# Performance work log

Measured on AMD Instinct MI355X. Metric: run time of the kernel, lower is better.

Reference implementation:

```python
import jax, jax.numpy as jnp
import numpy as np


def _conv1x1(w, b, x):
    # 1x1 Conv2d == channel matmul: w [O,C], x [B,C,H,W] -> [B,O,H,W]
    return jnp.einsum('oc,bchw->bohw', w, x) + b[None, :, None, None]


def setup_inputs() -> dict:
    key = jax.random.key(0)
    ks = jax.random.split(key, 9)
    C = 512
    B, H, W = 8, 32, 32
    s = 0.02
    return {
        'x': jax.random.normal(ks[0], (B, C, H, W), dtype=jnp.float32),
        'wq': jax.random.normal(ks[1], (C, C), dtype=jnp.float32) * s,
        'bq': jax.random.normal(ks[2], (C,), dtype=jnp.float32) * s,
        'wk': jax.random.normal(ks[3], (C, C), dtype=jnp.float32) * s,
        'bk': jax.random.normal(ks[4], (C,), dtype=jnp.float32) * s,
        'wv': jax.random.normal(ks[5], (C, C), dtype=jnp.float32) * s,
        'bv': jax.random.normal(ks[6], (C,), dtype=jnp.float32) * s,
        'wo': jax.random.normal(ks[7], (C, C), dtype=jnp.float32) * s,
        'bo': jax.random.normal(ks[8], (C,), dtype=jnp.float32) * s,
        'heads': 8,
    }


def reference(x, wq, bq, wk, bk, wv, bv, wo, bo, heads):
    B, C, H, W = x.shape
    N = H * W
    d = C // heads
    scale = jnp.asarray(d, x.dtype) ** 0.5

    vx = _conv1x1(wv, bv, x)                       # value(x), reused for residual
    Q = _conv1x1(wq, bq, x).reshape(B, heads, d, N)
    K = _conv1x1(wk, bk, x).reshape(B, heads, d, N)
    V = vx.reshape(B, heads, d, N)

    attn = jax.nn.softmax(jnp.einsum('bhcn,bhcm->bhnm', Q, K) / scale, axis=-1)
    attn_out = jnp.einsum('bhnm,bhcm->bhcn', attn, V).reshape(B, C, H, W)

    out = attn_out + vx                            # residual uses value(x)
    return _conv1x1(wo, bo, out)
```

## Files before the change

### kernel.cpp

```cpp
#include <hip/hip_runtime.h>
#include <cstdint>
#include <cmath>

#define B_ 8
#define C_ 512
#define N_ 1024
#define H_ 8
#define D_ 64


using u16 = unsigned short;

typedef __bf16 bf16x8 __attribute__((ext_vector_type(8)));
typedef float  f32x4  __attribute__((ext_vector_type(4)));
typedef unsigned short us8 __attribute__((ext_vector_type(8)));

#if __has_builtin(__builtin_amdgcn_exp2f)
#define EXP2(x) __builtin_amdgcn_exp2f(x)
#else
#define EXP2(x) exp2f(x)
#endif

#define QSCALE 0.1803368801111244f


__device__ __forceinline__ float b2f(u16 u) {
    return __uint_as_float(((uint32_t)u) << 16);
}
__device__ __forceinline__ u16 f2b(float f) {
    uint32_t x = __float_as_uint(f);
    return (u16)((x + 0x7fffu + ((x >> 16) & 1u)) >> 16);
}
__device__ __forceinline__ u16 f2bt(float f) {
    return (u16)(__float_as_uint(f) >> 16);
}
__device__ __forceinline__ float sf(float f) {
    return (fabsf(f) < 1e30f) ? f : 0.0f;
}
__device__ __forceinline__ u16 sf2b(float f) { return f2b(sf(f)); }

__device__ __forceinline__ void gl16(const void* g, const void* l) {
    __builtin_amdgcn_global_load_lds(
        (const __attribute__((address_space(1))) uint32_t*)g,
        (__attribute__((address_space(3))) uint32_t*)(uint32_t)(uintptr_t)l,
        16, 0, 0);
}

__device__ __forceinline__ us8 ldwf(const float* W, size_t idx) {
    const float* p = W + idx;
    float4 a = *(const float4*)p, b = *(const float4*)(p + 4);
    us8 pk;
    pk[0] = sf2b(a.x); pk[1] = sf2b(a.y); pk[2] = sf2b(a.z); pk[3] = sf2b(a.w);
    pk[4] = sf2b(b.x); pk[5] = sf2b(b.y); pk[6] = sf2b(b.z); pk[7] = sf2b(b.w);
    return pk;
}


__global__ __launch_bounds__(256) void k_pre(const float* __restrict__ x,
                                             u16* __restrict__ xt,
                                             const float* __restrict__ wq,
                                             const float* __restrict__ wk,
                                             const float* __restrict__ wv,
                                             const float* __restrict__ wo,
                                             u16* __restrict__ wb) {
    const int tid = threadIdx.x;
    const int nb = blockIdx.x, cb = blockIdx.y, b = blockIdx.z;
    if (b == 8) {
        if (wb == nullptr) return;
        int base = (cb * 16 + nb) * 256 + tid;
#pragma unroll
        for (int i = 0; i < 8; ++i) {
            int idx = base + i * 32768;
            int m = idx >> 16;
            int off = (idx & 65535) << 2;
            const float* src = (m == 0) ? wq : (m == 1) ? wk : (m == 2) ? wv : wo;
            float4 v = *(const float4*)&src[off];
            ushort4 w;
            w.x = sf2b(v.x); w.y = sf2b(v.y); w.z = sf2b(v.z); w.w = sf2b(v.w);
            *(ushort4*)&wb[(m << 18) + off] = w;
        }
        return;
    }
    __shared__ __align__(16) u16 t[64][72];
#pragma unroll
    for (int i = 0; i < 4; ++i) {
        int q = tid + i * 256;
        int row = q >> 4, cg = q & 15;
        float4 v = *(const float4*)&x[((size_t)(b * C_ + cb * 64 + row) << 10) + nb * 64 + cg * 4];
        ushort4 w;
        w.x = sf2b(v.x); w.y = sf2b(v.y); w.z = sf2b(v.z); w.w = sf2b(v.w);
        *(ushort4*)&t[row][cg * 4] = w;
    }
    __syncthreads();
#pragma unroll
    for (int i = 0; i < 4; ++i) {
        int q = tid + i * 256;
        int nrow = q >> 4, cg = q & 15;
        ushort4 w;
        w.x = t[cg * 4 + 0][nrow];
        w.y = t[cg * 4 + 1][nrow];
        w.z = t[cg * 4 + 2][nrow];
        w.w = t[cg * 4 + 3][nrow];
        *(ushort4*)&xt[((size_t)(b * N_ + nb * 64 + nrow) << 9) + cb * 64 + cg * 4] = w;
    }
}


template<bool WB>
__global__ __launch_bounds__(256) void k_proj_t(
    const u16* __restrict__ xt,
    const void* __restrict__ wq, const float* __restrict__ bq,
    const void* __restrict__ wk, const float* __restrict__ bk,
    const void* __restrict__ wv, const float* __restrict__ bv,
    u16* __restrict__ qt, u16* __restrict__ kt,
    u16* __restrict__ v,  u16* __restrict__ vxt) {
    __shared__ __align__(16) u16 lA[128 * 64];
    __shared__ __align__(16) u16 lB[128 * 64];
    const int tid = threadIdx.x;
    const int op = blockIdx.z >> 3, b = blockIdx.z & 7;
    const int n0 = blockIdx.x * 128, o0 = blockIdx.y * 128;
    const void*  W  = (op == 0) ? wq : (op == 1) ? wk : wv;
    const float* BI = (op == 0) ? bq : (op == 1) ? bk : bv;
    const u16* A = xt + ((size_t)b << 19);
    const int lane = tid & 63, wave = tid >> 6;
    const int wm = (wave >> 1) * 64, wn = (wave & 1) * 64;
    const int l15 = lane & 15, lg = lane >> 4;
    const int xs = (l15 & 7) << 3;

    f32x4 acc[4][4];
    const f32x4 vzero = {0.f, 0.f, 0.f, 0.f};
#pragma unroll
    for (int i = 0; i < 4; ++i)
#pragma unroll
        for (int j = 0; j < 4; ++j) acc[i][j] = vzero;

    us8 ra[4], rwB[4];
    auto loadk = [&](int k0) {
#pragma unroll
        for (int p = 0; p < 4; ++p) {
            int slot = p * 256 + tid;
            int row = slot >> 3, seg = slot & 7;
            ra[p] = *(const us8*)&A[(size_t)(n0 + row) * C_ + k0 + seg * 8];
            rwB[p] = ldwf((const float*)W, (size_t)(o0 + row) * C_ + k0 + seg * 8);
        }
    };
    if constexpr (!WB) loadk(0);

    for (int k0 = 0; k0 < C_; k0 += 64) {
        __syncthreads();
        if constexpr (WB) {
            const u16* W16 = (const u16*)W;
#pragma unroll
            for (int p = 0; p < 4; ++p) {
                int slot = p * 256 + tid;
                int row = slot >> 3;
                int segs = (slot & 7) ^ (row & 7);
                int lb = (p * 256 + (tid & 192)) * 8;
                gl16(&A[(size_t)(n0 + row) * C_ + k0 + segs * 8], &lA[lb]);
                gl16(&W16[(size_t)(o0 + row) * C_ + k0 + segs * 8], &lB[lb]);
            }
        } else {
#pragma unroll
            for (int p = 0; p < 4; ++p) {
                int slot = p * 256 + tid;
                int row = slot >> 3, seg = slot & 7;
                int off = row * 64 + ((seg ^ (row & 7)) << 3);
                *(us8*)&lA[off] = ra[p];
                *(us8*)&lB[off] = rwB[p];
            }
            if (k0 + 64 < C_) loadk(k0 + 64);
        }
        __syncthreads();
#pragma unroll
        for (int kk = 0; kk < 64; kk += 32) {
            const int col = (kk + lg * 8) ^ xs;
            bf16x8 af[4], bfr[4];
#pragma unroll
            for (int i = 0; i < 4; ++i)
                af[i] = *(const bf16x8*)&lA[(wm + i * 16 + l15) * 64 + col];
#pragma unroll
            for (int j = 0; j < 4; ++j)
                bfr[j] = *(const bf16x8*)&lB[(wn + j * 16 + l15) * 64 + col];
#pragma unroll
            for (int i = 0; i < 4; ++i)
#pragma unroll
                for (int j = 0; j < 4; ++j)
                    acc[i][j] = __builtin_amdgcn_mfma_f32_16x16x32_bf16(af[i], bfr[j], acc[i][j], 0, 0, 0);
        }
    }

    if (op < 2) {
        u16* outp = (op == 0) ? qt : kt;
        const float scl = (op == 0) ? QSCALE : 1.0f;
#pragma unroll
        for (int i = 0; i < 4; ++i) {
            int nb2 = n0 + wm + i * 16 + lg * 4;
#pragma unroll
            for (int j = 0; j < 4; ++j) {
                int o = o0 + wn + j * 16 + l15;
                float bias = sf(BI[o]);
                int h = o >> 6, dl = o & 63;
                size_t base = ((size_t)b * H_ + h) << 10;
#pragma unroll
                for (int r = 0; r < 4; ++r)
                    outp[(base + nb2 + r) * D_ + dl] = f2b((acc[i][j][r] + bias) * scl);
            }
        }
    } else {
#pragma unroll
        for (int i = 0; i < 4; ++i) {
            int nb2 = n0 + wm + i * 16 + lg * 4;
#pragma unroll
            for (int j = 0; j < 4; ++j) {
                int o = o0 + wn + j * 16 + l15;
                float bias = sf(BI[o]);
                float p0 = acc[i][j][0] + bias, p1 = acc[i][j][1] + bias;
                float p2 = acc[i][j][2] + bias, p3 = acc[i][j][3] + bias;
                ushort4 pk; pk.x = f2b(p0); pk.y = f2b(p1); pk.z = f2b(p2); pk.w = f2b(p3);
                *(ushort4*)&v[((size_t)(b * C_ + o) << 10) + nb2] = pk;
                vxt[((size_t)(b * N_ + nb2 + 0) << 9) + o] = pk.x;
                vxt[((size_t)(b * N_ + nb2 + 1) << 9) + o] = pk.y;
                vxt[((size_t)(b * N_ + nb2 + 2) << 9) + o] = pk.z;
                vxt[((size_t)(b * N_ + nb2 + 3) << 9) + o] = pk.w;
            }
        }
    }
}


__global__ __launch_bounds__(256, 3) void k_attn(
    const u16* __restrict__ qt, const u16* __restrict__ kt,
    const u16* __restrict__ v,  const u16* __restrict__ vxt,
    u16* __restrict__ rt) {
    __shared__ __align__(16) u16 lK[2][64 * 64];
    __shared__ __align__(16) u16 lV[2][64 * 64];
    __shared__ __align__(16) u16 lP[4][32 * 64];
    const int tid = threadIdx.x, lane = tid & 63, wave = tid >> 6;
    const int l15 = lane & 15, lg = lane >> 4;
    const int xs = (l15 & 7) << 3;
    const int bid = blockIdx.x;
    const int qb = bid >> 6, bh = bid & 63;
    const int b = bh >> 3, h = bh & 7;
    const size_t bh_off = (size_t)bh << 16;
    const int q0 = qb * 128;
    const int nA = wave * 32;

    bf16x8 qf[2][2];
#pragma unroll
    for (int nt = 0; nt < 2; ++nt)
#pragma unroll
        for (int k = 0; k < 2; ++k)
            qf[nt][k] = *(const bf16x8*)&qt[bh_off +
                (size_t)(q0 + nA + nt * 16 + l15) * D_ + k * 32 + lg * 8];

    auto stage = [&](int mb, int buf) {
#pragma unroll
        for (int p = 0; p < 2; ++p) {
            int slot = p * 256 + tid;
            int row = slot >> 3;
            int segs = (slot & 7) ^ (row & 7);
            int lb = (p * 256 + (tid & 192)) * 8;
            gl16(&kt[bh_off + (size_t)(mb * 64 + row) * D_ + segs * 8], &lK[buf][lb]);
            gl16(&v[((size_t)(b * C_ + h * 64 + row) << 10) + mb * 64 + segs * 8], &lV[buf][lb]);
        }
    };
    stage(0, 0);
    __syncthreads();

    float L[2] = {0.f, 0.f};
    f32x4 oacc[2][4];
    const f32x4 vzero = {0.f, 0.f, 0.f, 0.f};
#pragma unroll
    for (int nt = 0; nt < 2; ++nt)
#pragma unroll
        for (int ct = 0; ct < 4; ++ct) oacc[nt][ct] = vzero;

    for (int mb = 0; mb < 16; ++mb) {
        const int cur = mb & 1;
        if (mb < 15) stage(mb + 1, cur ^ 1);
        const u16* lKc = lK[cur];
        const u16* lVc = lV[cur];

        f32x4 s[4][2];
#pragma unroll
        for (int mt = 0; mt < 4; ++mt)
#pragma unroll
            for (int nt = 0; nt < 2; ++nt) s[mt][nt] = vzero;
#pragma unroll
        for (int k = 0; k < 2; ++k) {
            const int col = (k * 32 + lg * 8) ^ xs;
            bf16x8 aK[4];
#pragma unroll
            for (int mt = 0; mt < 4; ++mt)
                aK[mt] = *(const bf16x8*)&lKc[(mt * 16 + l15) * 64 + col];
            __builtin_amdgcn_s_setprio(1);
#pragma unroll
            for (int mt = 0; mt < 4; ++mt)
#pragma unroll
                for (int nt = 0; nt < 2; ++nt)
                    s[mt][nt] = __builtin_amdgcn_mfma_f32_16x16x32_bf16(aK[mt], qf[nt][k], s[mt][nt], 0, 0, 0);
            __builtin_amdgcn_s_setprio(0);
        }

#pragma unroll
        for (int mt = 0; mt < 4; ++mt)
#pragma unroll
            for (int nt = 0; nt < 2; ++nt) {
                float p0 = EXP2(s[mt][nt][0]);
                float p1 = EXP2(s[mt][nt][1]);
                float p2 = EXP2(s[mt][nt][2]);
                float p3 = EXP2(s[mt][nt][3]);
                L[nt] += p0 + p1 + p2 + p3;
                ushort4 pk; pk.x = f2bt(p0); pk.y = f2bt(p1); pk.z = f2bt(p2); pk.w = f2bt(p3);
                *(ushort4*)&lP[wave][(nt * 16 + l15) * 64 + ((mt * 16 + lg * 4) ^ xs)] = pk;
            }

#pragma unroll
        for (int kk2 = 0; kk2 < 64; kk2 += 32) {
            const int colv = (kk2 + lg * 8) ^ xs;
            bf16x8 aP[2], bV[4];
#pragma unroll
            for (int nt = 0; nt < 2; ++nt)
                aP[nt] = *(const bf16x8*)&lP[wave][(nt * 16 + l15) * 64 + colv];
#pragma unroll
            for (int ct = 0; ct < 4; ++ct)
                bV[ct] = *(const bf16x8*)&lVc[(ct * 16 + l15) * 64 + colv];
            __builtin_amdgcn_s_setprio(1);
#pragma unroll
            for (int nt = 0; nt < 2; ++nt)
#pragma unroll
                for (int ct = 0; ct < 4; ++ct)
                    oacc[nt][ct] = __builtin_amdgcn_mfma_f32_16x16x32_bf16(aP[nt], bV[ct], oacc[nt][ct], 0, 0, 0);
            __builtin_amdgcn_s_setprio(0);
        }

        __syncthreads();
    }

#pragma unroll
    for (int nt = 0; nt < 2; ++nt) {
        float s2 = L[nt];
        s2 += __shfl_xor(s2, 16);
        s2 += __shfl_xor(s2, 32);
        L[nt] = s2;
    }

#pragma unroll
    for (int nt = 0; nt < 2; ++nt) {
        float inv[4];
#pragma unroll
        for (int r = 0; r < 4; ++r) inv[r] = 1.0f / __shfl(L[nt], lg * 4 + r);
#pragma unroll
        for (int ct = 0; ct < 4; ++ct) {
            int ch = h * 64 + ct * 16 + l15;
#pragma unroll
            for (int r = 0; r < 4; ++r) {
                int n = q0 + nA + nt * 16 + lg * 4 + r;
                size_t idx = ((size_t)(b * N_ + n) << 9) + ch;
                rt[idx] = f2b(oacc[nt][ct][r] * inv[r] + b2f(vxt[idx]));
            }
        }
    }
}


template<bool WB>
__global__ __launch_bounds__(256) void k_out_t(
    const u16* __restrict__ rt, const void* __restrict__ wo,
    const float* __restrict__ bo, float* __restrict__ out) {
    __shared__ __align__(16) u16 lA[128 * 64];
    __shared__ __align__(16) u16 lB[128 * 64];
    const int tid = threadIdx.x;
    const int b = blockIdx.z;
    const int n0 = blockIdx.x * 128, o0 = blockIdx.y * 128;
    const u16* Rb = rt + ((size_t)b << 19);
    const int lane = tid & 63, wave = tid >> 6;
    const int wm = (wave >> 1) * 64, wn = (wave & 1) * 64;
    const int l15 = lane & 15, lg = lane >> 4;
    const int xs = (l15 & 7) << 3;

    f32x4 acc[4][4];
    const f32x4 vzero = {0.f, 0.f, 0.f, 0.f};
#pragma unroll
    for (int i = 0; i < 4; ++i)
#pragma unroll
        for (int j = 0; j < 4; ++j) acc[i][j] = vzero;

    us8 rb[4], rwB[4];
    auto loadk = [&](int k0) {
#pragma unroll
        for (int p = 0; p < 4; ++p) {
            int slot = p * 256 + tid;
            int row = slot >> 3, seg = slot & 7;
            rwB[p] = ldwf((const float*)wo, (size_t)(o0 + row) * C_ + k0 + seg * 8);
            rb[p] = *(const us8*)&Rb[(size_t)(n0 + row) * C_ + k0 + seg * 8];
        }
    };
    if constexpr (!WB) loadk(0);

    for (int k0 = 0; k0 < C_; k0 += 64) {
        __syncthreads();
        if constexpr (WB) {
            const u16* W16 = (const u16*)wo;
#pragma unroll
            for (int p = 0; p < 4; ++p) {
                int slot = p * 256 + tid;
                int row = slot >> 3;
                int segs = (slot & 7) ^ (row & 7);
                int lb = (p * 256 + (tid & 192)) * 8;
                gl16(&W16[(size_t)(o0 + row) * C_ + k0 + segs * 8], &lA[lb]);
                gl16(&Rb[(size_t)(n0 + row) * C_ + k0 + segs * 8], &lB[lb]);
            }
        } else {
#pragma unroll
            for (int p = 0; p < 4; ++p) {
                int slot = p * 256 + tid;
                int row = slot >> 3, seg = slot & 7;
                int off = row * 64 + ((seg ^ (row & 7)) << 3);
                *(us8*)&lA[off] = rwB[p];
                *(us8*)&lB[off] = rb[p];
            }
            if (k0 + 64 < C_) loadk(k0 + 64);
        }
        __syncthreads();
#pragma unroll
        for (int kk = 0; kk < 64; kk += 32) {
            const int col = (kk + lg * 8) ^ xs;
            bf16x8 af[4], bfr[4];
#pragma unroll
            for (int i = 0; i < 4; ++i)
                af[i] = *(const bf16x8*)&lA[(wm + i * 16 + l15) * 64 + col];
#pragma unroll
            for (int j = 0; j < 4; ++j)
                bfr[j] = *(const bf16x8*)&lB[(wn + j * 16 + l15) * 64 + col];
#pragma unroll
            for (int i = 0; i < 4; ++i)
#pragma unroll
                for (int j = 0; j < 4; ++j)
                    acc[i][j] = __builtin_amdgcn_mfma_f32_16x16x32_bf16(af[i], bfr[j], acc[i][j], 0, 0, 0);
        }
    }

#pragma unroll
    for (int i = 0; i < 4; ++i) {
#pragma unroll
        for (int j = 0; j < 4; ++j) {
            int nn = n0 + wn + j * 16 + l15;
#pragma unroll
            for (int r = 0; r < 4; ++r) {
                int o = o0 + wm + i * 16 + lg * 4 + r;
                out[((size_t)(b * C_ + o) << 10) + nn] = acc[i][j][r] + sf(bo[o]);
            }
        }
    }
}


extern "C" void kernel_launch(void* const* d_in, const int* in_sizes, int n_in,
                              void* d_out, int out_size, void* d_ws, size_t ws_size,
                              hipStream_t stream) {
    const float* x  = (const float*)d_in[0];
    const float* wq = (const float*)d_in[1];
    const float* bq = (const float*)d_in[2];
    const float* wk = (const float*)d_in[3];
    const float* bk = (const float*)d_in[4];
    const float* wv = (const float*)d_in[5];
    const float* bv = (const float*)d_in[6];
    const float* wo = (const float*)d_in[7];
    const float* bo = (const float*)d_in[8];
    float* out = (float*)d_out;
    u16* ws = (u16*)d_ws;

    const size_t T = (size_t)B_ * C_ * N_;
    const size_t WSZ = (size_t)4 * C_ * C_;
    if (ws_size < 5 * T * sizeof(u16)) return;

    u16* xt  = ws;
    u16* qt  = ws + 1 * T;
    u16* kt  = ws + 2 * T;
    u16* vv  = ws + 3 * T;
    u16* vxt = ws + 4 * T;
    u16* rt  = xt;
    u16* wb  = ws + 5 * T;

    const bool wbfit = ws_size >= (5 * T + WSZ) * sizeof(u16);

    k_pre<<<dim3(16, 8, 9), 256, 0, stream>>>(x, xt, wq, wk, wv, wo,
                                              wbfit ? wb : (u16*)nullptr);
    if (wbfit) {
        k_proj_t<true><<<dim3(8, 4, 24), 256, 0, stream>>>(
            xt, wb, bq, wb + 262144, bk, wb + 524288, bv, qt, kt, vv, vxt);
    } else {
        k_proj_t<false><<<dim3(8, 4, 24), 256, 0, stream>>>(
            xt, wq, bq, wk, bk, wv, bv, qt, kt, vv, vxt);
    }
    k_attn<<<dim3(512), 256, 0, stream>>>(qt, kt, vv, vxt, rt);
    if (wbfit) {
        k_out_t<true><<<dim3(8, 4, 8), 256, 0, stream>>>(rt, wb + 786432, bo, out);
    } else {
        k_out_t<false><<<dim3(8, 4, 8), 256, 0, stream>>>(rt, wo, bo, out);
    }
}
```

Before: 76.31 us.

## Switch attention kernel to 32x32x16 MFMA and keep P in registers

Rewrites the attention inner loop to use 32x32x16 bf16 MFMA tiles instead of 16x16x32. The softmax probabilities are packed and redistributed across lanes with cross-half shuffles, so P no longer round-trips through LDS. That removes the lP shared buffer and its writes and reads, and reduces LDS footprint. In exchange it adds shuffle and select overhead, uses larger accumulator register tiles, and depends on the lane layout mapping being exactly right.

```diff
diff --git a/kernel.cpp b/kernel.cpp
--- a/kernel.cpp
+++ b/kernel.cpp
@@ -13,7 +13,9 @@
 
 typedef __bf16 bf16x8 __attribute__((ext_vector_type(8)));
 typedef float  f32x4  __attribute__((ext_vector_type(4)));
+typedef float  f32x16 __attribute__((ext_vector_type(16)));
 typedef unsigned short us8 __attribute__((ext_vector_type(8)));
+typedef uint32_t u32x4 __attribute__((ext_vector_type(4)));
 
 #if __has_builtin(__builtin_amdgcn_exp2f)
 #define EXP2(x) __builtin_amdgcn_exp2f(x)
@@ -234,24 +236,21 @@
     u16* __restrict__ rt) {
     __shared__ __align__(16) u16 lK[2][64 * 64];
     __shared__ __align__(16) u16 lV[2][64 * 64];
-    __shared__ __align__(16) u16 lP[4][32 * 64];
     const int tid = threadIdx.x, lane = tid & 63, wave = tid >> 6;
-    const int l15 = lane & 15, lg = lane >> 4;
-    const int xs = (l15 & 7) << 3;
+    const int l31 = lane & 31, hi = lane >> 5;
+    const int xs = (l31 & 7) << 3;
     const int bid = blockIdx.x;
     const int qb = bid >> 6, bh = bid & 63;
     const int b = bh >> 3, h = bh & 7;
     const size_t bh_off = (size_t)bh << 16;
     const int q0 = qb * 128;
     const int nA = wave * 32;
-
-    bf16x8 qf[2][2];
-#pragma unroll
-    for (int nt = 0; nt < 2; ++nt)
-#pragma unroll
-        for (int k = 0; k < 2; ++k)
-            qf[nt][k] = *(const bf16x8*)&qt[bh_off +
-                (size_t)(q0 + nA + nt * 16 + l15) * D_ + k * 32 + lg * 8];
+    const int qrow = q0 + nA + l31;
+
+    bf16x8 qf[4];
+#pragma unroll
+    for (int kk = 0; kk < 4; ++kk)
+        qf[kk] = *(const bf16x8*)&qt[bh_off + (size_t)qrow * D_ + kk * 16 + hi * 8];
 
     auto stage = [&](int mb, int buf) {
 #pragma unroll
@@ -267,13 +266,12 @@
     stage(0, 0);
     __syncthreads();
 
-    float L[2] = {0.f, 0.f};
-    f32x4 oacc[2][4];
-    const f32x4 vzero = {0.f, 0.f, 0.f, 0.f};
-#pragma unroll
-    for (int nt = 0; nt < 2; ++nt)
-#pragma unroll
-        for (int ct = 0; ct < 4; ++ct) oacc[nt][ct] = vzero;
+    float L = 0.f;
+    f32x16 oacc[2];
+#pragma unroll
+    for (int ct = 0; ct < 2; ++ct)
+#pragma unroll
+        for (int e = 0; e < 16; ++e) oacc[ct][e] = 0.f;
 
     for (int mb = 0; mb < 16; ++mb) {
         const int cur = mb & 1;
@@ -281,84 +279,79 @@
         const u16* lKc = lK[cur];
         const u16* lVc = lV[cur];
 
-        f32x4 s[4][2];
-#pragma unroll
-        for (int mt = 0; mt < 4; ++mt)
-#pragma unroll
-            for (int nt = 0; nt < 2; ++nt) s[mt][nt] = vzero;
-#pragma unroll
-        for (int k = 0; k < 2; ++k) {
-            const int col = (k * 32 + lg * 8) ^ xs;
-            bf16x8 aK[4];
-#pragma unroll
-            for (int mt = 0; mt < 4; ++mt)
-                aK[mt] = *(const bf16x8*)&lKc[(mt * 16 + l15) * 64 + col];
+        f32x16 s[2];
+#pragma unroll
+        for (int mt = 0; mt < 2; ++mt)
+#pragma unroll
+            for (int e = 0; e < 16; ++e) s[mt][e] = 0.f;
+#pragma unroll
+        for (int kk = 0; kk < 4; ++kk) {
+            const int col = (kk * 16 + hi * 8) ^ xs;
+            bf16x8 k0 = *(const bf16x8*)&lKc[l31 * 64 + col];
+            bf16x8 k1 = *(const bf16x8*)&lKc[(32 + l31) * 64 + col];
             __builtin_amdgcn_s_setprio(1);
-#pragma unroll
-            for (int mt = 0; mt < 4; ++mt)
-#pragma unroll
-                for (int nt = 0; nt < 2; ++nt)
-                    s[mt][nt] = __builtin_amdgcn_mfma_f32_16x16x32_bf16(aK[mt], qf[nt][k], s[mt][nt], 0, 0, 0);
+            s[0] = __builtin_amdgcn_mfma_f32_32x32x16_bf16(k0, qf[kk], s[0], 0, 0, 0);
+            s[1] = __builtin_amdgcn_mfma_f32_32x32x16_bf16(k1, qf[kk], s[1], 0, 0, 0);
             __builtin_amdgcn_s_setprio(0);
         }
 
-#pragma unroll
-        for (int mt = 0; mt < 4; ++mt)
-#pragma unroll
-            for (int nt = 0; nt < 2; ++nt) {
-                float p0 = EXP2(s[mt][nt][0]);
-                float p1 = EXP2(s[mt][nt][1]);
-                float p2 = EXP2(s[mt][nt][2]);
-                float p3 = EXP2(s[mt][nt][3]);
-                L[nt] += p0 + p1 + p2 + p3;
-                ushort4 pk; pk.x = f2bt(p0); pk.y = f2bt(p1); pk.z = f2bt(p2); pk.w = f2bt(p3);
-                *(ushort4*)&lP[wave][(nt * 16 + l15) * 64 + ((mt * 16 + lg * 4) ^ xs)] = pk;
-            }
-
-#pragma unroll
-        for (int kk2 = 0; kk2 < 64; kk2 += 32) {
-            const int colv = (kk2 + lg * 8) ^ xs;
-            bf16x8 aP[2], bV[4];
-#pragma unroll
-            for (int nt = 0; nt < 2; ++nt)
-                aP[nt] = *(const bf16x8*)&lP[wave][(nt * 16 + l15) * 64 + colv];
-#pragma unroll
-            for (int ct = 0; ct < 4; ++ct)
-                bV[ct] = *(const bf16x8*)&lVc[(ct * 16 + l15) * 64 + colv];
+        uint32_t pk[2][4][2];
+#pragma unroll
+        for (int mt = 0; mt < 2; ++mt)
+#pragma unroll
+            for (int g = 0; g < 4; ++g) {
+                float e0 = EXP2(s[mt][4 * g + 0]);
+                float e1 = EXP2(s[mt][4 * g + 1]);
+                float e2 = EXP2(s[mt][4 * g + 2]);
+                float e3 = EXP2(s[mt][4 * g + 3]);
+                L += e0 + e1 + e2 + e3;
+                pk[mt][g][0] = (uint32_t)f2bt(e0) | ((uint32_t)f2bt(e1) << 16);
+                pk[mt][g][1] = (uint32_t)f2bt(e2) | ((uint32_t)f2bt(e3) << 16);
+            }
+
+#pragma unroll
+        for (int s2 = 0; s2 < 4; ++s2) {
+            const int mt = s2 >> 1, kl = s2 & 1;
+            const int ga = 2 * kl, gb = 2 * kl + 1;
+            uint32_t swa0 = (uint32_t)__shfl_xor((int)pk[mt][ga][0], 32);
+            uint32_t swa1 = (uint32_t)__shfl_xor((int)pk[mt][ga][1], 32);
+            uint32_t swb0 = (uint32_t)__shfl_xor((int)pk[mt][gb][0], 32);
+            uint32_t swb1 = (uint32_t)__shfl_xor((int)pk[mt][gb][1], 32);
+            u32x4 av;
+            av.x = hi ? swb0 : pk[mt][ga][0];
+            av.y = hi ? swb1 : pk[mt][ga][1];
+            av.z = hi ? pk[mt][gb][0] : swa0;
+            av.w = hi ? pk[mt][gb][1] : swa1;
+            union { u32x4 u; bf16x8 b; } cvt; cvt.u = av;
+            const int colv = (s2 * 16 + hi * 8) ^ xs;
+            bf16x8 v0 = *(const bf16x8*)&lVc[l31 * 64 + colv];
+            bf16x8 v1 = *(const bf16x8*)&lVc[(32 + l31) * 64 + colv];
             __builtin_amdgcn_s_setprio(1);
-#pragma unroll
-            for (int nt = 0; nt < 2; ++nt)
-#pragma unroll
-                for (int ct = 0; ct < 4; ++ct)
-                    oacc[nt][ct] = __builtin_amdgcn_mfma_f32_16x16x32_bf16(aP[nt], bV[ct], oacc[nt][ct], 0, 0, 0);
+            oacc[0] = __builtin_amdgcn_mfma_f32_32x32x16_bf16(cvt.b, v0, oacc[0], 0, 0, 0);
+            oacc[1] = __builtin_amdgcn_mfma_f32_32x32x16_bf16(cvt.b, v1, oacc[1], 0, 0, 0);
             __builtin_amdgcn_s_setprio(0);
         }
 
         __syncthreads();
     }
 
-#pragma unroll
-    for (int nt = 0; nt < 2; ++nt) {
-        float s2 = L[nt];
-        s2 += __shfl_xor(s2, 16);
-        s2 += __shfl_xor(s2, 32);
-        L[nt] = s2;
-    }
-
-#pragma unroll
-    for (int nt = 0; nt < 2; ++nt) {
-        float inv[4];
-#pragma unroll
-        for (int r = 0; r < 4; ++r) inv[r] = 1.0f / __shfl(L[nt], lg * 4 + r);
-#pragma unroll
-        for (int ct = 0; ct < 4; ++ct) {
-            int ch = h * 64 + ct * 16 + l15;
-#pragma unroll
-            for (int r = 0; r < 4; ++r) {
-                int n = q0 + nA + nt * 16 + lg * 4 + r;
-                size_t idx = ((size_t)(b * N_ + n) << 9) + ch;
-                rt[idx] = f2b(oacc[nt][ct][r] * inv[r] + b2f(vxt[idx]));
-            }
+    float Lf = L + __shfl_xor(L, 32);
+    float inv[16];
+#pragma unroll
+    for (int r = 0; r < 16; ++r) {
+        int nloc = (r & 3) + 8 * (r >> 2) + 4 * hi;
+        inv[r] = 1.0f / __shfl(Lf, nloc);
+    }
+
+#pragma unroll
+    for (int ct = 0; ct < 2; ++ct) {
+        int ch = h * 64 + ct * 32 + l31;
+#pragma unroll
+        for (int r = 0; r < 16; ++r) {
+            int nloc = (r & 3) + 8 * (r >> 2) + 4 * hi;
+            int n = q0 + nA + nloc;
+            size_t idx = ((size_t)(b * N_ + n) << 9) + ch;
+            rt[idx] = f2b(oacc[ct][r] * inv[r] + b2f(vxt[idx]));
         }
     }
 }
```

Result: slower. 80.69 us (+5.7%).
